# Optimization experiments

Measured on AMD Instinct MI355X. Metric: run time of the kernel, lower is better.

## Reference

```python
import jax, jax.numpy as jnp
import numpy as np

NUM_HEADS = 8
NUM_LAYERS = 4
BASE_THR = 0.5     # AdaptiveLIF base_threshold (state reset -> no adaptation on single step)
TAU_MEM = 5.0      # tau_mem (single step from zero state: mem = decay*0 + x = x)
SURR_SLOPE = 5.0   # fast-sigmoid surrogate slope (forward path unaffected)
EPS = 1e-5
NEG = -1e9


@jax.custom_vjp
def spike(u):
    return (u > 0.0).astype(u.dtype)

def _spike_fwd(u):
    return (u > 0.0).astype(u.dtype), u

def _spike_bwd(u, g):
    return (g / (1.0 + SURR_SLOPE * jnp.abs(u)) ** 2,)

spike.defvjp(_spike_fwd, _spike_bwd)


def lif(x):
    # AdaptiveLIF, single timestep from reset state: mem = x, thr = base_threshold
    return spike(x - BASE_THR)


def layer_norm(x, g, b):
    m = jnp.mean(x, axis=-1, keepdims=True)
    v = jnp.mean((x - m) ** 2, axis=-1, keepdims=True)
    return (x - m) * jax.lax.rsqrt(v + EPS) * g + b


def dsa(x, wq, bq, wk, bk, wv, bv, wo, bo, top_k):
    # Dynamic Sparse Attention: dense scores -> per-query top-k mask -> softmax -> AV
    B, T, D = x.shape
    H = NUM_HEADS
    dh = D // H

    def heads(w, bias):
        return (x @ w.T + bias).reshape(B, T, H, dh).transpose(0, 2, 1, 3)  # [B,H,T,dh]

    q, k, v = heads(wq, bq), heads(wk, bk), heads(wv, bv)
    scores = jnp.einsum('bhqd,bhkd->bhqk', q, k) / jnp.sqrt(jnp.asarray(dh, x.dtype))
    vals, idx = jax.lax.top_k(scores, top_k)  # [B,H,T,K]

    # scatter top-k values into a -inf-filled score matrix (exact top-k sparsity)
    N = B * H * T
    rows = jnp.arange(N)[:, None]
    sp = jnp.full((N, T), NEG, scores.dtype).at[rows, idx.reshape(N, top_k)].set(vals.reshape(N, top_k))
    attn = jax.nn.softmax(sp.reshape(B, H, T, T), axis=-1)

    out = jnp.einsum('bhqk,bhkd->bhqd', attn, v)
    out = out.transpose(0, 2, 1, 3).reshape(B, T, D)
    out = out @ wo.T + bo
    return lif(out)  # spiking output of attention


def ffn(x, w1, b1, w2, b2):
    h = lif(x @ w1.T + b1)
    return lif(h @ w2.T + b2)


def setup_inputs() -> dict:
    key = jax.random.key(0)
    ks = jax.random.split(key, 16)
    L, D, F, IN, OUT, B, T = NUM_LAYERS, 512, 2048, 128, 256, 2, 2048
    s = 0.02
    return {
        'x': jax.random.normal(ks[0], (B, T, IN), jnp.float32),
        'emb_w': jax.random.normal(ks[1], (D, IN), jnp.float32) * s,
        'emb_b': jnp.zeros((D,), jnp.float32),
        'pos_emb': jax.random.normal(ks[2], (1, T, D), jnp.float32) * s,
        'wq': jax.random.normal(ks[3], (L, D, D), jnp.float32) * s,
        'bq': jnp.zeros((L, D), jnp.float32),
        'wk': jax.random.normal(ks[4], (L, D, D), jnp.float32) * s,
        'bk': jnp.zeros((L, D), jnp.float32),
        'wv': jax.random.normal(ks[5], (L, D, D), jnp.float32) * s,
        'bv': jnp.zeros((L, D), jnp.float32),
        'wo': jax.random.normal(ks[6], (L, D, D), jnp.float32) * s,
        'bo': jnp.zeros((L, D), jnp.float32),
        'ln1_g': jnp.ones((L, D), jnp.float32),
        'ln1_b': jnp.zeros((L, D), jnp.float32),
        'fc1_w': jax.random.normal(ks[7], (L, F, D), jnp.float32) * s,
        'fc1_b': jnp.zeros((L, F), jnp.float32),
        'fc2_w': jax.random.normal(ks[8], (L, D, F), jnp.float32) * s,
        'fc2_b': jnp.zeros((L, D), jnp.float32),
        'ln2_g': jnp.ones((L, D), jnp.float32),
        'ln2_b': jnp.zeros((L, D), jnp.float32),
        'fnorm_g': jnp.ones((D,), jnp.float32),
        'fnorm_b': jnp.zeros((D,), jnp.float32),
        'cls_w': jax.random.normal(ks[9], (OUT, D), jnp.float32) * s,
        'cls_b': jnp.zeros((OUT,), jnp.float32),
        'top_k': 32,
    }


def reference(x, emb_w, emb_b, pos_emb, wq, bq, wk, bk, wv, bv, wo, bo,
              ln1_g, ln1_b, fc1_w, fc1_b, fc2_w, fc2_b, ln2_g, ln2_b,
              fnorm_g, fnorm_b, cls_w, cls_b, top_k):
    B, T, _ = x.shape
    h = x @ emb_w.T + emb_b + pos_emb[:, :T, :]
    for l in range(NUM_LAYERS):
        a = dsa(h, wq[l], bq[l], wk[l], bk[l], wv[l], bv[l], wo[l], bo[l], top_k)
        h = layer_norm(h + a, ln1_g[l], ln1_b[l])
        f = ffn(h, fc1_w[l], fc1_b[l], fc2_w[l], fc2_b[l])
        h = layer_norm(h + f, ln2_g[l], ln2_b[l])
    h = layer_norm(h, fnorm_g, fnorm_b)
    pooled = jnp.mean(h, axis=1)  # [B, D]
    return pooled @ cls_w.T + cls_b
```

## Files before the change

kernel.cpp:

```cpp
#include <hip/hip_runtime.h>
#include <math.h>
#include <float.h>

#define T_SEQ  2048
#define DMODEL 512
#define NHEAD  8
#define DHEAD  64
#define FDIM   2048
#define NLAYER 4
#define NB     2
#define MROWS  (NB*T_SEQ)

typedef _Float16 f16x8 __attribute__((ext_vector_type(8)));
typedef float    f32x4 __attribute__((ext_vector_type(4)));

template<int BN, int EPI, int LAYOUT>
__global__ __launch_bounds__(256) void gemm_k(
    const float* __restrict__ A, const float* __restrict__ W,
    const float* __restrict__ bias, const float* __restrict__ pos,
    float* __restrict__ C, int M, int N, int K)
{
    constexpr int BM = 128;
    constexpr int BK = 32;
    constexpr int MN = BN / 16;
    __shared__ float As[BK][BM + 4];
    __shared__ float Ws[BK][BN + 4];
    const int tid = threadIdx.x;
    const int n0 = blockIdx.x * BN;
    const int m0 = blockIdx.y * BM;
    const int tx = tid & 15;
    const int ty = tid >> 4;

    float acc[8][MN];
    #pragma unroll
    for (int i = 0; i < 8; ++i)
        #pragma unroll
        for (int j = 0; j < MN; ++j) acc[i][j] = 0.f;

    for (int k0 = 0; k0 < K; k0 += BK) {
        #pragma unroll
        for (int it = 0; it < 4; ++it) {
            int qq = tid + 256 * it;
            int m = qq >> 3, kq = qq & 7;
            float4 v4 = *(const float4*)(A + (size_t)(m0 + m) * K + k0 + kq * 4);
            As[kq*4+0][m] = v4.x; As[kq*4+1][m] = v4.y;
            As[kq*4+2][m] = v4.z; As[kq*4+3][m] = v4.w;
        }
        #pragma unroll
        for (int it = 0; it < BN/32; ++it) {
            int qq = tid + 256 * it;
            int n = qq >> 3, kq = qq & 7;
            float4 v4 = *(const float4*)(W + (size_t)(n0 + n) * K + k0 + kq * 4);
            Ws[kq*4+0][n] = v4.x; Ws[kq*4+1][n] = v4.y;
            Ws[kq*4+2][n] = v4.z; Ws[kq*4+3][n] = v4.w;
        }
        __syncthreads();
        for (int kk = 0; kk < BK; ++kk) {
            float a[8], b[MN];
            float4 a0 = *(const float4*)&As[kk][ty*8];
            float4 a1 = *(const float4*)&As[kk][ty*8+4];
            a[0]=a0.x; a[1]=a0.y; a[2]=a0.z; a[3]=a0.w;
            a[4]=a1.x; a[5]=a1.y; a[6]=a1.z; a[7]=a1.w;
            float4 b0 = *(const float4*)&Ws[kk][tx*4];
            b[0]=b0.x; b[1]=b0.y; b[2]=b0.z; b[3]=b0.w;
            if constexpr (MN == 8) {
                float4 b1 = *(const float4*)&Ws[kk][64 + tx*4];
                b[4]=b1.x; b[5]=b1.y; b[6]=b1.z; b[7]=b1.w;
            }
            #pragma unroll
            for (int i = 0; i < 8; ++i)
                #pragma unroll
                for (int j = 0; j < MN; ++j)
                    acc[i][j] = fmaf(a[i], b[j], acc[i][j]);
        }
        __syncthreads();
    }

    #pragma unroll
    for (int i = 0; i < 8; ++i) {
        int m = m0 + ty*8 + i;
        #pragma unroll
        for (int jb = 0; jb < MN/4; ++jb) {
            int nn = n0 + jb*64 + tx*4;
            float4 r;
            r.x = acc[i][jb*4+0] + bias[nn+0];
            r.y = acc[i][jb*4+1] + bias[nn+1];
            r.z = acc[i][jb*4+2] + bias[nn+2];
            r.w = acc[i][jb*4+3] + bias[nn+3];
            if constexpr (EPI == 1) {
                const float* pp = pos + (size_t)(m & (T_SEQ-1)) * DMODEL + nn;
                r.x += pp[0]; r.y += pp[1]; r.z += pp[2]; r.w += pp[3];
            }
            if constexpr (EPI == 2) {
                r.x = r.x > 0.5f ? 1.f : 0.f;
                r.y = r.y > 0.5f ? 1.f : 0.f;
                r.z = r.z > 0.5f ? 1.f : 0.f;
                r.w = r.w > 0.5f ? 1.f : 0.f;
            }
            *(float4*)(C + (size_t)m * N + nn) = r;
        }
    }
}

template<int ASRC, int EPI, int LAYOUT>
__global__ __launch_bounds__(256, 2) void mgemm_k(
    const _Float16* __restrict__ AH, const _Float16* __restrict__ AL,
    const _Float16* __restrict__ WH, const _Float16* __restrict__ WL,
    const float* __restrict__ bias,
    float* __restrict__ O0, float* __restrict__ O1, float* __restrict__ O2,
    float* __restrict__ O3, float* __restrict__ O4,
    int M, int N, int K)
{
    __shared__ _Float16 AsH[4][128][8];
    __shared__ _Float16 AsL[4][128][8];
    __shared__ _Float16 WsH[4][128][8];
    __shared__ _Float16 WsL[4][128][8];

    const int tid = threadIdx.x;
    const int n0 = blockIdx.x * 128;
    const int m0 = blockIdx.y * 128;
    const int wv = tid >> 6, lane = tid & 63;
    const int mw = (wv >> 1) * 64, nw = (wv & 1) * 64;
    const int fr = lane & 15;
    const int kb = lane >> 4;

    const int srow = tid >> 1;
    const int skoff = (tid & 1) * 16;
    const int skb = skoff >> 3;

    f32x4 acc[4][4];
    #pragma unroll
    for (int i = 0; i < 4; ++i)
        #pragma unroll
        for (int j = 0; j < 4; ++j) acc[i][j] = (f32x4)(0.f);

    for (int k0 = 0; k0 < K; k0 += 32) {
        {
            const _Float16* ap = AH + (size_t)(m0 + srow) * K + k0 + skoff;
            *(f16x8*)&AsH[skb  ][srow][0] = *(const f16x8*)ap;
            *(f16x8*)&AsH[skb+1][srow][0] = *(const f16x8*)(ap + 8);
            if constexpr (ASRC == 0) {
                const _Float16* alp = AL + (size_t)(m0 + srow) * K + k0 + skoff;
                *(f16x8*)&AsL[skb  ][srow][0] = *(const f16x8*)alp;
                *(f16x8*)&AsL[skb+1][srow][0] = *(const f16x8*)(alp + 8);
            }
        }
        {
            const _Float16* wp = WH + (size_t)(n0 + srow) * K + k0 + skoff;
            *(f16x8*)&WsH[skb  ][srow][0] = *(const f16x8*)wp;
            *(f16x8*)&WsH[skb+1][srow][0] = *(const f16x8*)(wp + 8);
            const _Float16* wlp = WL + (size_t)(n0 + srow) * K + k0 + skoff;
            *(f16x8*)&WsL[skb  ][srow][0] = *(const f16x8*)wlp;
            *(f16x8*)&WsL[skb+1][srow][0] = *(const f16x8*)(wlp + 8);
        }
        __syncthreads();

        f16x8 aH[4], aL[4], bH[4], bL[4];
        #pragma unroll
        for (int i = 0; i < 4; ++i) {
            aH[i] = *(const f16x8*)&AsH[kb][mw + i*16 + fr][0];
            if constexpr (ASRC == 0) aL[i] = *(const f16x8*)&AsL[kb][mw + i*16 + fr][0];
            bH[i] = *(const f16x8*)&WsH[kb][nw + i*16 + fr][0];
            bL[i] = *(const f16x8*)&WsL[kb][nw + i*16 + fr][0];
        }
        #pragma unroll
        for (int i = 0; i < 4; ++i)
            #pragma unroll
            for (int j = 0; j < 4; ++j) {
                acc[i][j] = __builtin_amdgcn_mfma_f32_16x16x32_f16(aH[i], bH[j], acc[i][j], 0, 0, 0);
                acc[i][j] = __builtin_amdgcn_mfma_f32_16x16x32_f16(aH[i], bL[j], acc[i][j], 0, 0, 0);
                if constexpr (ASRC == 0)
                    acc[i][j] = __builtin_amdgcn_mfma_f32_16x16x32_f16(aL[i], bH[j], acc[i][j], 0, 0, 0);
            }
        __syncthreads();
    }

    const int q = lane >> 4;
    #pragma unroll
    for (int j = 0; j < 4; ++j) {
        int n = n0 + nw + j*16 + fr;
        float bv = bias[n];
        #pragma unroll
        for (int i = 0; i < 4; ++i) {
            #pragma unroll
            for (int r = 0; r < 4; ++r) {
                int m = m0 + mw + i*16 + q*4 + r;
                float val = acc[i][j][r] * (1.f/1024.f) + bv;
                if constexpr (EPI == 2) val = val > 0.5f ? 1.f : 0.f;
                if constexpr (EPI == 3) {
                    ((_Float16*)O0)[(size_t)m * N + n] = (val > 0.5f) ? (_Float16)16.f : (_Float16)0.f;
                } else if constexpr (LAYOUT == 0) {
                    O0[(size_t)m * N + n] = val;
                } else {
                    int b_ = m >> 11, t_ = m & (T_SEQ-1);
                    if (n < 512) {
                        size_t hl = (((size_t)(b_*NHEAD + (n>>6))*T_SEQ + t_) << 6) + (n & 63);
                        float s16 = 16.f * val;
                        _Float16 hh = (_Float16)s16;
                        ((_Float16*)O0)[hl] = hh;
                        ((_Float16*)O1)[hl] = (_Float16)(s16 - (float)hh);
                    } else if (n < 1024) {
                        int nn = n - 512;
                        size_t hl = (((size_t)(b_*NHEAD + (nn>>6))*T_SEQ + t_) << 6) + (nn & 63);
                        float s16 = 16.f * val;
                        _Float16 hh = (_Float16)s16;
                        ((_Float16*)O2)[hl] = hh;
                        ((_Float16*)O3)[hl] = (_Float16)(s16 - (float)hh);
                    } else {
                        int nn = n - 1024;
                        O4[(((size_t)(b_*NHEAD + (nn>>6))*T_SEQ + t_) << 6) + (nn & 63)] = val;
                    }
                }
            }
        }
    }
}

__global__ __launch_bounds__(256) void cvtw_k(
    const float* __restrict__ w, _Float16* __restrict__ H, _Float16* __restrict__ L,
    int n, float scale)
{
    int i = blockIdx.x * 256 + threadIdx.x;
    if (i < n) {
        float s = scale * w[i];
        _Float16 h = (_Float16)s;
        H[i] = h;
        L[i] = (_Float16)(s - (float)h);
    }
}

__global__ __launch_bounds__(256) void cat_k(
    const float* __restrict__ wq, const float* __restrict__ wk, const float* __restrict__ wv,
    const float* __restrict__ bq, const float* __restrict__ bk, const float* __restrict__ bv,
    _Float16* __restrict__ WH, _Float16* __restrict__ WL, float* __restrict__ bcat)
{
    int i = blockIdx.x * 256 + threadIdx.x;
    if (i < 786432) {
        int src = i >> 18, off = i & 262143;
        float w = (src == 0 ? wq : (src == 1 ? wk : wv))[off];
        float s = 64.f * w;
        _Float16 h = (_Float16)s;
        WH[i] = h;
        WL[i] = (_Float16)(s - (float)h);
    } else if (i < 786432 + 1536) {
        int j = i - 786432;
        int src = j >> 9, off = j & 511;
        bcat[j] = (src == 0 ? bq : (src == 1 ? bk : bv))[off];
    }
}

__global__ __launch_bounds__(256) void attn_k(
    const _Float16* __restrict__ qH, const _Float16* __restrict__ qL,
    const _Float16* __restrict__ kH, const _Float16* __restrict__ kL,
    const float* __restrict__ v,
    _Float16* __restrict__ outH, _Float16* __restrict__ outL)
{
    __shared__ unsigned char lds[46080];
    _Float16 (*ksH)[72] = (_Float16(*)[72])(lds);
    _Float16 (*ksL)[72] = (_Float16(*)[72])(lds + 18432);
    _Float16 (*qsH)[72] = (_Float16(*)[72])(lds + 36864);
    _Float16 (*qsL)[72] = (_Float16(*)[72])(lds + 41472);
    float    (*ss)[132] = (float(*)[132])(lds);
    float*   wrow       = (float*)(lds);
    int*     irow       = (int*)(lds + 4224);

    const int tid = threadIdx.x;
    const int bh  = blockIdx.y;
    const int t0  = blockIdx.x * 32;
    const _Float16* qHb = qH + ((size_t)bh * T_SEQ + t0) * DHEAD;
    const _Float16* qLb = qL + ((size_t)bh * T_SEQ + t0) * DHEAD;
    const _Float16* kHb = kH + (size_t)bh * T_SEQ * DHEAD;
    const _Float16* kLb = kL + (size_t)bh * T_SEQ * DHEAD;
    const float*    vb  = v  + (size_t)bh * T_SEQ * DHEAD;

    {
        int r = tid >> 3, c = tid & 7;
        *(f16x8*)&qsH[r][c*8] = *(const f16x8*)(qHb + r*DHEAD + c*8);
        *(f16x8*)&qsL[r][c*8] = *(const f16x8*)(qLb + r*DHEAD + c*8);
    }

    unsigned kreg[32];
    #pragma unroll
    for (int i = 0; i < 32; ++i) kreg[i] = 0u;

    const int wv = tid >> 6, lane = tid & 63;
    const int fr = lane & 15, q4 = lane >> 4;
    const int c0w = wv * 32;
    const int srow = tid >> 3;
    const int ssub = tid & 7;

    for (int jt = 0; jt < 16; ++jt) {
        const int j0 = jt * 128;
        {
            int c = tid & 7, r0 = tid >> 3;
            #pragma unroll
            for (int it = 0; it < 4; ++it) {
                int r = r0 + 32*it;
                *(f16x8*)&ksH[r][c*8] = *(const f16x8*)(kHb + (size_t)(j0 + r)*DHEAD + c*8);
                *(f16x8*)&ksL[r][c*8] = *(const f16x8*)(kLb + (size_t)(j0 + r)*DHEAD + c*8);
            }
        }
        __syncthreads();

        f32x4 acc[2][2];
        acc[0][0] = (f32x4)(0.f); acc[0][1] = (f32x4)(0.f);
        acc[1][0] = (f32x4)(0.f); acc[1][1] = (f32x4)(0.f);
        #pragma unroll
        for (int ks = 0; ks < 2; ++ks) {
            const int doff = ks*32 + q4*8;
            f16x8 aH0 = *(const f16x8*)&qsH[fr][doff];
            f16x8 aH1 = *(const f16x8*)&qsH[16 + fr][doff];
            f16x8 aL0 = *(const f16x8*)&qsL[fr][doff];
            f16x8 aL1 = *(const f16x8*)&qsL[16 + fr][doff];
            #pragma unroll
            for (int nj = 0; nj < 2; ++nj) {
                const int cc = c0w + nj*16 + fr;
                f16x8 bHf = *(const f16x8*)&ksH[cc][doff];
                f16x8 bLf = *(const f16x8*)&ksL[cc][doff];
                acc[0][nj] = __builtin_amdgcn_mfma_f32_16x16x32_f16(aH0, bHf, acc[0][nj], 0, 0, 0);
                acc[0][nj] = __builtin_amdgcn_mfma_f32_16x16x32_f16(aH0, bLf, acc[0][nj], 0, 0, 0);
                acc[0][nj] = __builtin_amdgcn_mfma_f32_16x16x32_f16(aL0, bHf, acc[0][nj], 0, 0, 0);
                acc[1][nj] = __builtin_amdgcn_mfma_f32_16x16x32_f16(aH1, bHf, acc[1][nj], 0, 0, 0);
                acc[1][nj] = __builtin_amdgcn_mfma_f32_16x16x32_f16(aH1, bLf, acc[1][nj], 0, 0, 0);
                acc[1][nj] = __builtin_amdgcn_mfma_f32_16x16x32_f16(aL1, bHf, acc[1][nj], 0, 0, 0);
            }
        }
        __syncthreads();

        #pragma unroll
        for (int mi = 0; mi < 2; ++mi)
            #pragma unroll
            for (int nj = 0; nj < 2; ++nj)
                #pragma unroll
                for (int r = 0; r < 4; ++r)
                    ss[mi*16 + q4*4 + r][c0w + nj*16 + fr] = acc[mi][nj][r] * (1.f/2048.f);
        __syncthreads();

        float4 c4[4];
        {
            const float* ssr = &ss[srow][0] + ssub*4;
            #pragma unroll
            for (int g = 0; g < 4; ++g) c4[g] = *(const float4*)(ssr + g*32);
        }
        unsigned cand[16];
        #pragma unroll
        for (int g = 0; g < 4; ++g) {
            float vg[4] = {c4[g].x, c4[g].y, c4[g].z, c4[g].w};
            #pragma unroll
            for (int r = 0; r < 4; ++r) {
                unsigned u = __float_as_uint(vg[r]);
                u ^= (unsigned)((int)u >> 31) | 0x80000000u;
                int col = ssub*4 + g*32 + r;
                cand[g*4+r] = (u & 0xFFFFF800u) | (unsigned)(2047 - (j0 + col));
            }
        }
        #pragma unroll
        for (int k2 = 2; k2 <= 16; k2 <<= 1) {
            #pragma unroll
            for (int j2 = k2 >> 1; j2 > 0; j2 >>= 1) {
                #pragma unroll
                for (int i2 = 0; i2 < 16; ++i2) {
                    int l2 = i2 ^ j2;
                    if (l2 > i2) {
                        unsigned a = cand[i2], b = cand[l2];
                        bool sw = ((i2 & k2) == 0) ? (a < b) : (a > b);
                        cand[i2] = sw ? b : a;
                        cand[l2] = sw ? a : b;
                    }
                }
            }
        }
        #pragma unroll
        for (int j2 = 0; j2 < 16; ++j2) {
            unsigned b = cand[15 - j2];
            if (kreg[16 + j2] < b) kreg[16 + j2] = b;
        }
        #pragma unroll
        for (int st = 16; st >= 1; st >>= 1) {
            #pragma unroll
            for (int i2 = 0; i2 < 32; ++i2) {
                if ((i2 & st) == 0) {
                    unsigned lo = kreg[i2], hi = kreg[i2 | st];
                    kreg[i2]      = lo < hi ? hi : lo;
                    kreg[i2 | st] = lo < hi ? lo : hi;
                }
            }
        }
        __syncthreads();
    }

    #pragma unroll
    for (int s = 1; s <= 4; s <<= 1) {
        #pragma unroll
        for (int i = 0; i < 16; ++i) {
            unsigned pa = (unsigned)__shfl_xor((int)kreg[31-i], s, 64);
            unsigned pb = (unsigned)__shfl_xor((int)kreg[i],    s, 64);
            if (pa > kreg[i])    kreg[i]    = pa;
            if (pb > kreg[31-i]) kreg[31-i] = pb;
        }
        #pragma unroll
        for (int st = 16; st >= 1; st >>= 1) {
            #pragma unroll
            for (int i2 = 0; i2 < 32; ++i2) {
                if ((i2 & st) == 0) {
                    unsigned lo = kreg[i2], hi = kreg[i2 | st];
                    kreg[i2]      = lo < hi ? hi : lo;
                    kreg[i2 | st] = lo < hi ? lo : hi;
                }
            }
        }
    }

    if (ssub == 0) {
        float w[32];
        #pragma unroll
        for (int i = 0; i < 32; ++i) {
            unsigned um = kreg[i] & 0xFFFFF800u;
            unsigned ub = (um & 0x80000000u) ? (um ^ 0x80000000u) : ~um;
            w[i] = __uint_as_float(ub);
        }
        float m = w[0];
        float s = 0.f;
        #pragma unroll
        for (int i = 0; i < 32; ++i) { w[i] = expf(w[i] - m); s += w[i]; }
        float inv = 1.f / s;
        #pragma unroll
        for (int i = 0; i < 32; ++i) {
            wrow[srow*33 + i] = w[i] * inv;
            irow[srow*33 + i] = 2047 - (int)(kreg[i] & 0x7FFu);
        }
    }
    __syncthreads();

    const int wid = tid >> 6, lane2 = tid & 63;
    const int b = bh >> 3, h = bh & 7;
    for (int rr = wid; rr < 32; rr += 4) {
        float accv = 0.f;
        #pragma unroll
        for (int i = 0; i < 32; ++i) {
            float wgt = wrow[rr*33 + i];
            int   idx = irow[rr*33 + i];
            accv = fmaf(wgt, vb[(size_t)idx * DHEAD + lane2], accv);
        }
        size_t oi = ((size_t)(b * T_SEQ + t0 + rr)) * DMODEL + h * DHEAD + lane2;
        float s16 = 16.f * accv;
        _Float16 hh = (_Float16)s16;
        outH[oi] = hh;
        outL[oi] = (_Float16)(s16 - (float)hh);
    }
}

__global__ __launch_bounds__(256) void ln_k(
    const float* __restrict__ x, const float* __restrict__ res,
    const float* __restrict__ g, const float* __restrict__ bb,
    float* __restrict__ out, _Float16* __restrict__ oH, _Float16* __restrict__ oL)
{
    __shared__ float red[8];
    const int row = blockIdx.x;
    const int tid = threadIdx.x;
    const float* xr = x + (size_t)row * DMODEL;
    float v0 = xr[tid], v1 = xr[tid + 256];
    if (res) {
        const float* rr = res + (size_t)row * DMODEL;
        v0 += rr[tid]; v1 += rr[tid + 256];
    }
    float s = v0 + v1;
    #pragma unroll
    for (int o = 1; o < 64; o <<= 1) s += __shfl_xor(s, o);
    const int wid = tid >> 6, lane = tid & 63;
    if (lane == 0) red[wid] = s;
    __syncthreads();
    float mean = (red[0] + red[1] + red[2] + red[3]) * (1.f / DMODEL);
    float d0 = v0 - mean, d1 = v1 - mean;
    float qs = d0*d0 + d1*d1;
    #pragma unroll
    for (int o = 1; o < 64; o <<= 1) qs += __shfl_xor(qs, o);
    if (lane == 0) red[4 + wid] = qs;
    __syncthreads();
    float var = (red[4] + red[5] + red[6] + red[7]) * (1.f / DMODEL);
    float rs = rsqrtf(var + 1e-5f);
    float o0 = d0 * rs * g[tid]       + bb[tid];
    float o1 = d1 * rs * g[tid + 256] + bb[tid + 256];
    size_t base = (size_t)row * DMODEL;
    out[base + tid]       = o0;
    out[base + tid + 256] = o1;
    float s0 = 16.f * o0, s1 = 16.f * o1;
    _Float16 h0 = (_Float16)s0, h1 = (_Float16)s1;
    oH[base + tid]       = h0;
    oH[base + tid + 256] = h1;
    oL[base + tid]       = (_Float16)(s0 - (float)h0);
    oL[base + tid + 256] = (_Float16)(s1 - (float)h1);
}

__global__ __launch_bounds__(256) void pool_k(
    const float* __restrict__ h, float* __restrict__ part)
{
    const int chunk = blockIdx.x & 15;
    const int idx = (blockIdx.x >> 4) * 256 + threadIdx.x;
    const int b = idx >> 9, d = idx & 511;
    const float* p = h + ((size_t)b * T_SEQ + chunk * 128) * DMODEL + d;
    float s = 0.f;
    for (int t = 0; t < 128; ++t) s += p[(size_t)t * DMODEL];
    part[chunk * 1024 + idx] = s;
}

__global__ __launch_bounds__(256) void poolsum_k(
    const float* __restrict__ part, float* __restrict__ pooled)
{
    int idx = blockIdx.x * 256 + threadIdx.x;
    float s = 0.f;
    #pragma unroll
    for (int c = 0; c < 16; ++c) s += part[c * 1024 + idx];
    pooled[idx] = s * (1.f / T_SEQ);
}

__global__ __launch_bounds__(256) void cls_k(
    const float* __restrict__ pooled, const float* __restrict__ w,
    const float* __restrict__ bias, float* __restrict__ out)
{
    const int wid = threadIdx.x >> 6, lane = threadIdx.x & 63;
    const int oi = blockIdx.x * 4 + wid;
    const int b = oi >> 8, o = oi & 255;
    const float* pr = pooled + b * DMODEL;
    const float* wr = w + (size_t)o * DMODEL;
    float s = 0.f;
    for (int d = lane; d < DMODEL; d += 64) s = fmaf(pr[d], wr[d], s);
    #pragma unroll
    for (int off = 1; off < 64; off <<= 1) s += __shfl_xor(s, off);
    if (lane == 0) out[oi] = s + bias[o];
}

extern "C" void kernel_launch(void* const* d_in, const int* in_sizes, int n_in,
                              void* d_out, int out_size, void* d_ws, size_t ws_size,
                              hipStream_t stream)
{
    const float* x     = (const float*)d_in[0];
    const float* emb_w = (const float*)d_in[1];
    const float* emb_b = (const float*)d_in[2];
    const float* pos   = (const float*)d_in[3];
    const float* wq    = (const float*)d_in[4];
    const float* bq    = (const float*)d_in[5];
    const float* wk    = (const float*)d_in[6];
    const float* bk    = (const float*)d_in[7];
    const float* wv    = (const float*)d_in[8];
    const float* bv    = (const float*)d_in[9];
    const float* wo    = (const float*)d_in[10];
    const float* bo    = (const float*)d_in[11];
    const float* ln1g  = (const float*)d_in[12];
    const float* ln1b  = (const float*)d_in[13];
    const float* fc1w  = (const float*)d_in[14];
    const float* fc1b  = (const float*)d_in[15];
    const float* fc2w  = (const float*)d_in[16];
    const float* fc2b  = (const float*)d_in[17];
    const float* ln2g  = (const float*)d_in[18];
    const float* ln2b  = (const float*)d_in[19];
    const float* fng   = (const float*)d_in[20];
    const float* fnb   = (const float*)d_in[21];
    const float* clsw  = (const float*)d_in[22];
    const float* clsb  = (const float*)d_in[23];

    float* ws = (float*)d_ws;
    const size_t SZ  = (size_t)MROWS * DMODEL;
    const size_t HP  = SZ / 2;
    float*     h     = ws;
    float*     t1    = ws + 1*SZ;
    _Float16*  hH    = (_Float16*)(ws + 2*SZ);
    _Float16*  hL    = (_Float16*)(ws + 2*SZ + HP);
    _Float16*  aoH   = (_Float16*)(ws + 3*SZ);
    _Float16*  aoL   = (_Float16*)(ws + 3*SZ + HP);
    _Float16*  qbH   = (_Float16*)(ws + 4*SZ);
    _Float16*  qbL   = (_Float16*)(ws + 4*SZ + HP);
    _Float16*  kbH   = (_Float16*)(ws + 5*SZ);
    _Float16*  kbL   = (_Float16*)(ws + 5*SZ + HP);
    float*     vbuf  = ws + 6*SZ;
    _Float16*  WcatH = (_Float16*)(ws + 7*SZ);
    _Float16*  WcatL = (_Float16*)(ws + 7*SZ + 393216);
    _Float16*  WoH   = (_Float16*)(ws + 7*SZ + 786432);
    _Float16*  WoL   = (_Float16*)(ws + 7*SZ + 917504);
    _Float16*  W1H   = (_Float16*)(ws + 7*SZ + 1048576);
    _Float16*  W1L   = (_Float16*)(ws + 7*SZ + 1572864);
    _Float16*  W2H   = (_Float16*)(ws + 7*SZ + 2097152);
    _Float16*  W2L   = (_Float16*)(ws + 7*SZ + 2621440);
    float*     bcat  = ws + 7*SZ + 3145728;
    float*     pooled= ws + 7*SZ + 3145728 + 1536;
    float*     part  = ws + 7*SZ + 3145728 + 1536 + 1024;
    _Float16*  hid   = (_Float16*)(ws + 4*SZ);
    const size_t needed = (7*SZ + 3145728 + 1536 + 1024 + 16384) * sizeof(float);
    if (ws_size < needed) return;

    dim3 blk(256);

    gemm_k<64,1,0><<<dim3(DMODEL/64, MROWS/128), blk, 0, stream>>>(
        x, emb_w, emb_b, pos, h, MROWS, DMODEL, 128);
    cvtw_k<<<dim3((int)(SZ/256)), blk, 0, stream>>>(h, hH, hL, (int)SZ, 16.f);

    for (int l = 0; l < NLAYER; ++l) {
        const float* wq_l = wq + (size_t)l*DMODEL*DMODEL;
        const float* bq_l = bq + (size_t)l*DMODEL;
        const float* wk_l = wk + (size_t)l*DMODEL*DMODEL;
        const float* bk_l = bk + (size_t)l*DMODEL;
        const float* wv_l = wv + (size_t)l*DMODEL*DMODEL;
        const float* bv_l = bv + (size_t)l*DMODEL;
        const float* wo_l = wo + (size_t)l*DMODEL*DMODEL;
        const float* bo_l = bo + (size_t)l*DMODEL;
        const float* f1w_l = fc1w + (size_t)l*FDIM*DMODEL;
        const float* f1b_l = fc1b + (size_t)l*FDIM;
        const float* f2w_l = fc2w + (size_t)l*DMODEL*FDIM;
        const float* f2b_l = fc2b + (size_t)l*DMODEL;

        cat_k<<<dim3(3079), blk, 0, stream>>>(wq_l, wk_l, wv_l, bq_l, bk_l, bv_l,
                                              WcatH, WcatL, bcat);
        cvtw_k<<<dim3(1024), blk, 0, stream>>>(wo_l, WoH, WoL, 262144, 64.f);
        cvtw_k<<<dim3(4096), blk, 0, stream>>>(f1w_l, W1H, W1L, 1048576, 64.f);
        cvtw_k<<<dim3(4096), blk, 0, stream>>>(f2w_l, W2H, W2L, 1048576, 64.f);

        mgemm_k<0,0,2><<<dim3(12, 32), blk, 0, stream>>>(
            hH, hL, WcatH, WcatL, bcat,
            (float*)qbH, (float*)qbL, (float*)kbH, (float*)kbL, vbuf,
            MROWS, 1536, DMODEL);

        attn_k<<<dim3(T_SEQ/32, NB*NHEAD), blk, 0, stream>>>(
            qbH, qbL, kbH, kbL, vbuf, aoH, aoL);

        mgemm_k<0,2,0><<<dim3(4, 32), blk, 0, stream>>>(
            aoH, aoL, WoH, WoL, bo_l, t1, nullptr, nullptr, nullptr, nullptr,
            MROWS, DMODEL, DMODEL);
        ln_k<<<dim3(MROWS), blk, 0, stream>>>(h, t1, ln1g + (size_t)l*DMODEL,
                                              ln1b + (size_t)l*DMODEL, h, hH, hL);

        mgemm_k<0,3,0><<<dim3(16, 32), blk, 0, stream>>>(
            hH, hL, W1H, W1L, f1b_l, (float*)hid, nullptr, nullptr, nullptr, nullptr,
            MROWS, FDIM, DMODEL);
        mgemm_k<1,2,0><<<dim3(4, 32), blk, 0, stream>>>(
            hid, nullptr, W2H, W2L, f2b_l, t1, nullptr, nullptr, nullptr, nullptr,
            MROWS, DMODEL, FDIM);
        ln_k<<<dim3(MROWS), blk, 0, stream>>>(h, t1, ln2g + (size_t)l*DMODEL,
                                              ln2b + (size_t)l*DMODEL, h, hH, hL);
    }

    ln_k<<<dim3(MROWS), blk, 0, stream>>>(h, nullptr, fng, fnb, h, hH, hL);
    pool_k<<<dim3(64), blk, 0, stream>>>(h, part);
    poolsum_k<<<dim3(4), blk, 0, stream>>>(part, pooled);
    cls_k<<<dim3(128), blk, 0, stream>>>(pooled, clsw, clsb, (float*)d_out);
}
```

Before: 1.298 ms.

## Add async K prefetch in attention, BM=64 GEMM tiles, fuse weight conversions

The attention kernel now stages K tiles straight into LDS with global_load_lds, using an XOR-swizzled layout. It issues the next tile's load right after the score write, so the copy overlaps the top-k and softmax work, and the separate K-score region lets it drop one barrier. The mfma GEMM gains a BM template parameter, and the narrow-N GEMMs (QKV, out-proj, fc2) now use 64-row tiles to launch twice as many blocks on the GPU. The four per-layer weight-conversion launches are merged into one kernel. The attention LDS footprint grows, which may reduce occupancy.

```diff
diff --git a/kernel.cpp b/kernel.cpp
--- a/kernel.cpp
+++ b/kernel.cpp
@@ -14,7 +14,13 @@
 typedef _Float16 f16x8 __attribute__((ext_vector_type(8)));
 typedef float    f32x4 __attribute__((ext_vector_type(4)));
 
-template<int BN, int EPI, int LAYOUT>
+__device__ __forceinline__ void async16(const _Float16* g, _Float16* l) {
+    __builtin_amdgcn_global_load_lds(
+        (const __attribute__((address_space(1))) unsigned int*)g,
+        (__attribute__((address_space(3))) unsigned int*)l, 16, 0, 0);
+}
+
+template<int BN, int EPI>
 __global__ __launch_bounds__(256) void gemm_k(
     const float* __restrict__ A, const float* __restrict__ W,
     const float* __restrict__ bias, const float* __restrict__ pos,
@@ -91,18 +97,12 @@
                 const float* pp = pos + (size_t)(m & (T_SEQ-1)) * DMODEL + nn;
                 r.x += pp[0]; r.y += pp[1]; r.z += pp[2]; r.w += pp[3];
             }
-            if constexpr (EPI == 2) {
-                r.x = r.x > 0.5f ? 1.f : 0.f;
-                r.y = r.y > 0.5f ? 1.f : 0.f;
-                r.z = r.z > 0.5f ? 1.f : 0.f;
-                r.w = r.w > 0.5f ? 1.f : 0.f;
-            }
             *(float4*)(C + (size_t)m * N + nn) = r;
         }
     }
 }
 
-template<int ASRC, int EPI, int LAYOUT>
+template<int BM, int ASRC, int EPI, int LAYOUT>
 __global__ __launch_bounds__(256, 2) void mgemm_k(
     const _Float16* __restrict__ AH, const _Float16* __restrict__ AL,
     const _Float16* __restrict__ WH, const _Float16* __restrict__ WL,
@@ -111,60 +111,71 @@
     float* __restrict__ O3, float* __restrict__ O4,
     int M, int N, int K)
 {
-    __shared__ _Float16 AsH[4][128][8];
-    __shared__ _Float16 AsL[4][128][8];
+    constexpr int MI = BM / 32;
+    __shared__ _Float16 AsH[4][BM][8];
+    __shared__ _Float16 AsL[4][BM][8];
     __shared__ _Float16 WsH[4][128][8];
     __shared__ _Float16 WsL[4][128][8];
 
     const int tid = threadIdx.x;
     const int n0 = blockIdx.x * 128;
-    const int m0 = blockIdx.y * 128;
+    const int m0 = blockIdx.y * BM;
     const int wv = tid >> 6, lane = tid & 63;
-    const int mw = (wv >> 1) * 64, nw = (wv & 1) * 64;
+    const int mw = (wv >> 1) * (BM/2), nw = (wv & 1) * 64;
     const int fr = lane & 15;
     const int kb = lane >> 4;
 
-    const int srow = tid >> 1;
-    const int skoff = (tid & 1) * 16;
-    const int skb = skoff >> 3;
-
-    f32x4 acc[4][4];
-    #pragma unroll
-    for (int i = 0; i < 4; ++i)
+    const int wsrow = tid >> 1;
+    const int wskb  = (tid & 1) * 2;
+    const int wkoff = (tid & 1) * 16;
+
+    f32x4 acc[MI][4];
+    #pragma unroll
+    for (int i = 0; i < MI; ++i)
         #pragma unroll
         for (int j = 0; j < 4; ++j) acc[i][j] = (f32x4)(0.f);
 
     for (int k0 = 0; k0 < K; k0 += 32) {
+        if constexpr (BM == 128) {
+            const _Float16* ap = AH + (size_t)(m0 + wsrow) * K + k0 + wkoff;
+            *(f16x8*)&AsH[wskb  ][wsrow][0] = *(const f16x8*)ap;
+            *(f16x8*)&AsH[wskb+1][wsrow][0] = *(const f16x8*)(ap + 8);
+            if constexpr (ASRC == 0) {
+                const _Float16* alp = AL + (size_t)(m0 + wsrow) * K + k0 + wkoff;
+                *(f16x8*)&AsL[wskb  ][wsrow][0] = *(const f16x8*)alp;
+                *(f16x8*)&AsL[wskb+1][wsrow][0] = *(const f16x8*)(alp + 8);
+            }
+        } else {
+            const int arow = tid >> 2, akb = tid & 3;
+            *(f16x8*)&AsH[akb][arow][0] =
+                *(const f16x8*)(AH + (size_t)(m0 + arow) * K + k0 + akb*8);
+            if constexpr (ASRC == 0)
+                *(f16x8*)&AsL[akb][arow][0] =
+                    *(const f16x8*)(AL + (size_t)(m0 + arow) * K + k0 + akb*8);
+        }
         {
-            const _Float16* ap = AH + (size_t)(m0 + srow) * K + k0 + skoff;
-            *(f16x8*)&AsH[skb  ][srow][0] = *(const f16x8*)ap;
-            *(f16x8*)&AsH[skb+1][srow][0] = *(const f16x8*)(ap + 8);
-            if constexpr (ASRC == 0) {
-                const _Float16* alp = AL + (size_t)(m0 + srow) * K + k0 + skoff;
-                *(f16x8*)&AsL[skb  ][srow][0] = *(const f16x8*)alp;
-                *(f16x8*)&AsL[skb+1][srow][0] = *(const f16x8*)(alp + 8);
-            }
-        }
-        {
-            const _Float16* wp = WH + (size_t)(n0 + srow) * K + k0 + skoff;
-            *(f16x8*)&WsH[skb  ][srow][0] = *(const f16x8*)wp;
-            *(f16x8*)&WsH[skb+1][srow][0] = *(const f16x8*)(wp + 8);
-            const _Float16* wlp = WL + (size_t)(n0 + srow) * K + k0 + skoff;
-            *(f16x8*)&WsL[skb  ][srow][0] = *(const f16x8*)wlp;
-            *(f16x8*)&WsL[skb+1][srow][0] = *(const f16x8*)(wlp + 8);
+            const _Float16* wp = WH + (size_t)(n0 + wsrow) * K + k0 + wkoff;
+            *(f16x8*)&WsH[wskb  ][wsrow][0] = *(const f16x8*)wp;
+            *(f16x8*)&WsH[wskb+1][wsrow][0] = *(const f16x8*)(wp + 8);
+            const _Float16* wlp = WL + (size_t)(n0 + wsrow) * K + k0 + wkoff;
+            *(f16x8*)&WsL[wskb  ][wsrow][0] = *(const f16x8*)wlp;
+            *(f16x8*)&WsL[wskb+1][wsrow][0] = *(const f16x8*)(wlp + 8);
         }
         __syncthreads();
 
-        f16x8 aH[4], aL[4], bH[4], bL[4];
-        #pragma unroll
-        for (int i = 0; i < 4; ++i) {
+        f16x8 aH[MI], aL[MI], bH[4], bL[4];
+        #pragma unroll
+        for (int i = 0; i < MI; ++i) {
             aH[i] = *(const f16x8*)&AsH[kb][mw + i*16 + fr][0];
             if constexpr (ASRC == 0) aL[i] = *(const f16x8*)&AsL[kb][mw + i*16 + fr][0];
-            bH[i] = *(const f16x8*)&WsH[kb][nw + i*16 + fr][0];
-            bL[i] = *(const f16x8*)&WsL[kb][nw + i*16 + fr][0];
-        }
-        #pragma unroll
-        for (int i = 0; i < 4; ++i)
+        }
+        #pragma unroll
+        for (int j = 0; j < 4; ++j) {
+            bH[j] = *(const f16x8*)&WsH[kb][nw + j*16 + fr][0];
+            bL[j] = *(const f16x8*)&WsL[kb][nw + j*16 + fr][0];
+        }
+        #pragma unroll
+        for (int i = 0; i < MI; ++i)
             #pragma unroll
             for (int j = 0; j < 4; ++j) {
                 acc[i][j] = __builtin_amdgcn_mfma_f32_16x16x32_f16(aH[i], bH[j], acc[i][j], 0, 0, 0);
@@ -175,16 +186,16 @@
         __syncthreads();
     }
 
-    const int q = lane >> 4;
+    const int qq = lane >> 4;
     #pragma unroll
     for (int j = 0; j < 4; ++j) {
         int n = n0 + nw + j*16 + fr;
         float bv = bias[n];
         #pragma unroll
-        for (int i = 0; i < 4; ++i) {
+        for (int i = 0; i < MI; ++i) {
             #pragma unroll
             for (int r = 0; r < 4; ++r) {
-                int m = m0 + mw + i*16 + q*4 + r;
+                int m = m0 + mw + i*16 + qq*4 + r;
                 float val = acc[i][j][r] * (1.f/1024.f) + bv;
                 if constexpr (EPI == 2) val = val > 0.5f ? 1.f : 0.f;
                 if constexpr (EPI == 3) {
@@ -229,24 +240,39 @@
     }
 }
 
-__global__ __launch_bounds__(256) void cat_k(
+__global__ __launch_bounds__(256) void cvtlayer_k(
     const float* __restrict__ wq, const float* __restrict__ wk, const float* __restrict__ wv,
     const float* __restrict__ bq, const float* __restrict__ bk, const float* __restrict__ bv,
-    _Float16* __restrict__ WH, _Float16* __restrict__ WL, float* __restrict__ bcat)
+    const float* __restrict__ wo, const float* __restrict__ f1w, const float* __restrict__ f2w,
+    _Float16* __restrict__ WcatH, _Float16* __restrict__ WcatL, float* __restrict__ bcat,
+    _Float16* __restrict__ WoH, _Float16* __restrict__ WoL,
+    _Float16* __restrict__ W1H, _Float16* __restrict__ W1L,
+    _Float16* __restrict__ W2H, _Float16* __restrict__ W2L)
 {
     int i = blockIdx.x * 256 + threadIdx.x;
+    float w;
+    _Float16 *H, *L;
+    int off;
     if (i < 786432) {
-        int src = i >> 18, off = i & 262143;
-        float w = (src == 0 ? wq : (src == 1 ? wk : wv))[off];
-        float s = 64.f * w;
-        _Float16 h = (_Float16)s;
-        WH[i] = h;
-        WL[i] = (_Float16)(s - (float)h);
-    } else if (i < 786432 + 1536) {
-        int j = i - 786432;
-        int src = j >> 9, off = j & 511;
-        bcat[j] = (src == 0 ? bq : (src == 1 ? bk : bv))[off];
-    }
+        int src = i >> 18, o = i & 262143;
+        w = (src == 0 ? wq : (src == 1 ? wk : wv))[o];
+        H = WcatH; L = WcatL; off = i;
+    } else if (i < 1048576) {
+        off = i - 786432;  w = wo[off];  H = WoH; L = WoL;
+    } else if (i < 2097152) {
+        off = i - 1048576; w = f1w[off]; H = W1H; L = W1L;
+    } else if (i < 3145728) {
+        off = i - 2097152; w = f2w[off]; H = W2H; L = W2L;
+    } else if (i < 3145728 + 1536) {
+        int j = i - 3145728;
+        int src = j >> 9, o = j & 511;
+        bcat[j] = (src == 0 ? bq : (src == 1 ? bk : bv))[o];
+        return;
+    } else return;
+    float s = 64.f * w;
+    _Float16 h = (_Float16)s;
+    H[off] = h;
+    L[off] = (_Float16)(s - (float)h);
 }
 
 __global__ __launch_bounds__(256) void attn_k(
@@ -255,14 +281,14 @@
     const float* __restrict__ v,
     _Float16* __restrict__ outH, _Float16* __restrict__ outL)
 {
-    __shared__ unsigned char lds[46080];
-    _Float16 (*ksH)[72] = (_Float16(*)[72])(lds);
-    _Float16 (*ksL)[72] = (_Float16(*)[72])(lds + 18432);
-    _Float16 (*qsH)[72] = (_Float16(*)[72])(lds + 36864);
-    _Float16 (*qsL)[72] = (_Float16(*)[72])(lds + 41472);
-    float    (*ss)[132] = (float(*)[132])(lds);
-    float*   wrow       = (float*)(lds);
-    int*     irow       = (int*)(lds + 4224);
+    __shared__ unsigned char lds[58880];
+    _Float16* ksH = (_Float16*)(lds);
+    _Float16* ksL = (_Float16*)(lds + 16384);
+    _Float16 (*qsH)[72] = (_Float16(*)[72])(lds + 32768);
+    _Float16 (*qsL)[72] = (_Float16(*)[72])(lds + 37376);
+    float    (*ss)[132] = (float(*)[132])(lds + 41984);
+    float*   wrow       = (float*)(lds + 41984);
+    int*     irow       = (int*)(lds + 41984 + 4224);
 
     const int tid = threadIdx.x;
     const int bh  = blockIdx.y;
@@ -289,18 +315,24 @@
     const int srow = tid >> 3;
     const int ssub = tid & 7;
 
+    auto stage = [&](int jt) {
+        const int j0 = jt * 128;
+        #pragma unroll
+        for (int i = 0; i < 4; ++i) {
+            const int r0 = wv*32 + i*8;
+            const int cc = r0 + (lane >> 3);
+            const int ch = (lane & 7) ^ (cc & 7);
+            const size_t goff = (size_t)(j0 + cc) * DHEAD + ch*8;
+            async16(kHb + goff, ksH + r0*64);
+            async16(kLb + goff, ksL + r0*64);
+        }
+    };
+
+    stage(0);
+    __syncthreads();
+
     for (int jt = 0; jt < 16; ++jt) {
         const int j0 = jt * 128;
-        {
-            int c = tid & 7, r0 = tid >> 3;
-            #pragma unroll
-            for (int it = 0; it < 4; ++it) {
-                int r = r0 + 32*it;
-                *(f16x8*)&ksH[r][c*8] = *(const f16x8*)(kHb + (size_t)(j0 + r)*DHEAD + c*8);
-                *(f16x8*)&ksL[r][c*8] = *(const f16x8*)(kLb + (size_t)(j0 + r)*DHEAD + c*8);
-            }
-        }
-        __syncthreads();
 
         f32x4 acc[2][2];
         acc[0][0] = (f32x4)(0.f); acc[0][1] = (f32x4)(0.f);
@@ -308,6 +340,7 @@
         #pragma unroll
         for (int ks = 0; ks < 2; ++ks) {
             const int doff = ks*32 + q4*8;
+            const int chq  = ks*4 + q4;
             f16x8 aH0 = *(const f16x8*)&qsH[fr][doff];
             f16x8 aH1 = *(const f16x8*)&qsH[16 + fr][doff];
             f16x8 aL0 = *(const f16x8*)&qsL[fr][doff];
@@ -315,8 +348,9 @@
             #pragma unroll
             for (int nj = 0; nj < 2; ++nj) {
                 const int cc = c0w + nj*16 + fr;
-                f16x8 bHf = *(const f16x8*)&ksH[cc][doff];
-                f16x8 bLf = *(const f16x8*)&ksL[cc][doff];
+                const int sl = cc*64 + (chq ^ (cc & 7))*8;
+                f16x8 bHf = *(const f16x8*)&ksH[sl];
+                f16x8 bLf = *(const f16x8*)&ksL[sl];
                 acc[0][nj] = __builtin_amdgcn_mfma_f32_16x16x32_f16(aH0, bHf, acc[0][nj], 0, 0, 0);
                 acc[0][nj] = __builtin_amdgcn_mfma_f32_16x16x32_f16(aH0, bLf, acc[0][nj], 0, 0, 0);
                 acc[0][nj] = __builtin_amdgcn_mfma_f32_16x16x32_f16(aL0, bHf, acc[0][nj], 0, 0, 0);
@@ -325,8 +359,6 @@
                 acc[1][nj] = __builtin_amdgcn_mfma_f32_16x16x32_f16(aL1, bHf, acc[1][nj], 0, 0, 0);
             }
         }
-        __syncthreads();
-
         #pragma unroll
         for (int mi = 0; mi < 2; ++mi)
             #pragma unroll
@@ -335,6 +367,8 @@
                 for (int r = 0; r < 4; ++r)
                     ss[mi*16 + q4*4 + r][c0w + nj*16 + fr] = acc[mi][nj][r] * (1.f/2048.f);
         __syncthreads();
+
+        if (jt < 15) stage(jt + 1);
 
         float4 c4[4];
         {
@@ -590,7 +624,7 @@
 
     dim3 blk(256);
 
-    gemm_k<64,1,0><<<dim3(DMODEL/64, MROWS/128), blk, 0, stream>>>(
+    gemm_k<64,1><<<dim3(DMODEL/64, MROWS/128), blk, 0, stream>>>(
         x, emb_w, emb_b, pos, h, MROWS, DMODEL, 128);
     cvtw_k<<<dim3((int)(SZ/256)), blk, 0, stream>>>(h, hH, hL, (int)SZ, 16.f);
 
@@ -608,13 +642,11 @@
         const float* f2w_l = fc2w + (size_t)l*DMODEL*FDIM;
         const float* f2b_l = fc2b + (size_t)l*DMODEL;
 
-        cat_k<<<dim3(3079), blk, 0, stream>>>(wq_l, wk_l, wv_l, bq_l, bk_l, bv_l,
-                                              WcatH, WcatL, bcat);
-        cvtw_k<<<dim3(1024), blk, 0, stream>>>(wo_l, WoH, WoL, 262144, 64.f);
-        cvtw_k<<<dim3(4096), blk, 0, stream>>>(f1w_l, W1H, W1L, 1048576, 64.f);
-        cvtw_k<<<dim3(4096), blk, 0, stream>>>(f2w_l, W2H, W2L, 1048576, 64.f);
-
-        mgemm_k<0,0,2><<<dim3(12, 32), blk, 0, stream>>>(
+        cvtlayer_k<<<dim3(12294), blk, 0, stream>>>(
+            wq_l, wk_l, wv_l, bq_l, bk_l, bv_l, wo_l, f1w_l, f2w_l,
+            WcatH, WcatL, bcat, WoH, WoL, W1H, W1L, W2H, W2L);
+
+        mgemm_k<64,0,0,2><<<dim3(12, 64), blk, 0, stream>>>(
             hH, hL, WcatH, WcatL, bcat,
             (float*)qbH, (float*)qbL, (float*)kbH, (float*)kbL, vbuf,
             MROWS, 1536, DMODEL);
@@ -622,16 +654,16 @@
         attn_k<<<dim3(T_SEQ/32, NB*NHEAD), blk, 0, stream>>>(
             qbH, qbL, kbH, kbL, vbuf, aoH, aoL);
 
-        mgemm_k<0,2,0><<<dim3(4, 32), blk, 0, stream>>>(
+        mgemm_k<64,0,2,0><<<dim3(4, 64), blk, 0, stream>>>(
             aoH, aoL, WoH, WoL, bo_l, t1, nullptr, nullptr, nullptr, nullptr,
             MROWS, DMODEL, DMODEL);
         ln_k<<<dim3(MROWS), blk, 0, stream>>>(h, t1, ln1g + (size_t)l*DMODEL,
                                               ln1b + (size_t)l*DMODEL, h, hH, hL);
 
-        mgemm_k<0,3,0><<<dim3(16, 32), blk, 0, stream>>>(
+        mgemm_k<128,0,3,0><<<dim3(16, 32), blk, 0, stream>>>(
             hH, hL, W1H, W1L, f1b_l, (float*)hid, nullptr, nullptr, nullptr, nullptr,
             MROWS, FDIM, DMODEL);
-        mgemm_k<1,2,0><<<dim3(4, 32), blk, 0, stream>>>(
+        mgemm_k<64,1,2,0><<<dim3(4, 64), blk, 0, stream>>>(
             hid, nullptr, W2H, W2L, f2b_l, t1, nullptr, nullptr, nullptr, nullptr,
             MROWS, DMODEL, FDIM);
         ln_k<<<dim3(MROWS), blk, 0, stream>>>(h, t1, ln2g + (size_t)l*DMODEL,
```

New measurement: 1.231 ms. 1.05x faster.
